# Optimization experiments

Hardware: AMD Instinct MI355X
Metric: run time of the kernel (lower is better)

## Reference

```python
import jax, jax.numpy as jnp
import numpy as np

D_MODEL = 1024
HEADS = 4
HDIM = 64


def setup_inputs() -> dict:
    key = jax.random.key(0)
    k_x, k_qw, k_qb, k_kw, k_kb, k_hw = jax.random.split(key, 6)
    hidden_states = jax.random.normal(k_x, (2, 4096, D_MODEL), dtype=jnp.float32)
    # xavier_uniform bound for Linear(d_model -> heads*hdim)
    fan_out = HEADS * HDIM
    bound = float(np.sqrt(6.0 / (D_MODEL + fan_out)))
    q_weight = jax.random.uniform(k_qw, (fan_out, D_MODEL), minval=-bound, maxval=bound, dtype=jnp.float32)
    k_weight = jax.random.uniform(k_kw, (fan_out, D_MODEL), minval=-bound, maxval=bound, dtype=jnp.float32)
    # nn.Linear default bias init: U(-1/sqrt(fan_in), 1/sqrt(fan_in))
    b_bound = float(1.0 / np.sqrt(D_MODEL))
    q_bias = jax.random.uniform(k_qb, (fan_out,), minval=-b_bound, maxval=b_bound, dtype=jnp.float32)
    k_bias = jax.random.uniform(k_kb, (fan_out,), minval=-b_bound, maxval=b_bound, dtype=jnp.float32)
    indexer_weights = jax.random.normal(k_hw, (HEADS,), dtype=jnp.float32) * 0.1
    return {
        "hidden_states": hidden_states,
        "q_weight": q_weight,
        "q_bias": q_bias,
        "k_weight": k_weight,
        "k_bias": k_bias,
        "indexer_weights": indexer_weights,
    }


def reference(hidden_states, q_weight, q_bias, k_weight, k_bias, indexer_weights):
    b, s, _ = hidden_states.shape
    # Linear projections: x @ W^T + b  -> [b, s, heads*hdim]
    q = hidden_states @ q_weight.T + q_bias
    k = hidden_states @ k_weight.T + k_bias
    q = q.reshape(b, s, HEADS, HDIM)  # [b, s, h, d]
    k = k.reshape(b, s, HEADS, HDIM)
    # per-head QK^T -> [b, h, s, s]
    scores = jnp.einsum("bqhd,bkhd->bhqk", q, k)
    scores = jax.nn.relu(scores)
    # weighted sum over heads -> [b, s, s]
    index_scores = jnp.einsum("bhqk,h->bqk", scores, indexer_weights)
    return index_scores
```

## Files before the change

kernel.cpp:

```cpp
#include <hip/hip_runtime.h>


typedef __bf16 bf16;
typedef __bf16 bf16x4 __attribute__((ext_vector_type(4)));
typedef __bf16 bf16x8 __attribute__((ext_vector_type(8)));
typedef float f32x4 __attribute__((ext_vector_type(4)));

#define NB 2
#define SEQ 4096
#define DMODEL 1024
#define NHEAD 4
#define HDIM 64
#define NPROJ 256
#define MTOT 8192

__device__ __forceinline__ void async16(const void* g, void* l) {
  __builtin_amdgcn_global_load_lds(
      (const __attribute__((address_space(1))) void*)g,
      (__attribute__((address_space(3))) void*)l, 16, 0, 0);
}

__global__ __launch_bounds__(256) void k_convert(const float* __restrict__ wq,
                                                 const float* __restrict__ wk,
                                                 bf16* __restrict__ wqb,
                                                 bf16* __restrict__ wkb) {
  int i = blockIdx.x * 256 + threadIdx.x;
  float4 a = ((const float4*)wq)[i];
  bf16x4 oa = {(bf16)a.x, (bf16)a.y, (bf16)a.z, (bf16)a.w};
  ((bf16x4*)wqb)[i] = oa;
  float4 b = ((const float4*)wk)[i];
  bf16x4 ob = {(bf16)b.x, (bf16)b.y, (bf16)b.z, (bf16)b.w};
  ((bf16x4*)wkb)[i] = ob;
}

__global__ __launch_bounds__(256, 4) void k_proj(
    const float* __restrict__ x, const bf16* __restrict__ wqb,
    const bf16* __restrict__ wkb, const float* __restrict__ qbias,
    const float* __restrict__ kbias, bf16* __restrict__ Qb,
    bf16* __restrict__ Kb) {
  __shared__ __align__(16) bf16 As[64 * 72];
  __shared__ __align__(16) bf16 Bs[128 * 64];
  const int t = threadIdx.x;
  const int lane = t & 63, w = t >> 6;
  const int m16 = lane & 15, q = lane >> 4;
  const int m0 = blockIdx.x * 64;
  const int z = blockIdx.y;
  const int nh = blockIdx.z;
  const bf16* __restrict__ W = z ? wkb : wqb;

  f32x4 acc[4][2];
#pragma unroll
  for (int i = 0; i < 4; i++)
#pragma unroll
    for (int j = 0; j < 2; j++) acc[i][j] = {0.f, 0.f, 0.f, 0.f};

  for (int kt = 0; kt < 16; kt++) {
#pragma unroll
    for (int p = 0; p < 4; p++) {
      int n0 = w * 32 + p * 8;
      int r = n0 + (lane >> 3);
      int c = (lane & 7) ^ (r & 7);
      async16(W + (size_t)(nh * 128 + r) * DMODEL + kt * 64 + c * 8,
              Bs + n0 * 64);
    }
#pragma unroll
    for (int p = 0; p < 4; p++) {
      int r = p * 16 + (t >> 4);
      int c = (t & 15) * 4;
      float4 v = *(const float4*)(x + (size_t)(m0 + r) * DMODEL + kt * 64 + c);
      bf16x4 o = {(bf16)v.x, (bf16)v.y, (bf16)v.z, (bf16)v.w};
      *(bf16x4*)(As + r * 72 + c) = o;
    }
    __builtin_amdgcn_s_waitcnt(0);
    __syncthreads();

#pragma unroll
    for (int s = 0; s < 2; s++) {
      bf16x8 a[4], b[2];
#pragma unroll
      for (int mt = 0; mt < 4; mt++)
        a[mt] = *(const bf16x8*)(As + (mt * 16 + m16) * 72 + s * 32 + q * 8);
#pragma unroll
      for (int nt = 0; nt < 2; nt++) {
        int n = w * 32 + nt * 16 + m16;
        int cc = (4 * s + q) ^ (n & 7);
        b[nt] = *(const bf16x8*)(Bs + n * 64 + cc * 8);
      }
#pragma unroll
      for (int mt = 0; mt < 4; mt++)
#pragma unroll
        for (int nt = 0; nt < 2; nt++)
          acc[mt][nt] = __builtin_amdgcn_mfma_f32_16x16x32_bf16(
              a[mt], b[nt], acc[mt][nt], 0, 0, 0);
    }
    __syncthreads();
  }

  const float* __restrict__ bias = z ? kbias : qbias;
  bf16* __restrict__ outp = z ? Kb : Qb;
#pragma unroll
  for (int nt = 0; nt < 2; nt++) {
    int col = nh * 128 + w * 32 + nt * 16 + m16;
    float bv = bias[col];
#pragma unroll
    for (int mt = 0; mt < 4; mt++) {
      int row0 = m0 + mt * 16 + q * 4;
#pragma unroll
      for (int e = 0; e < 4; e++)
        outp[(size_t)(row0 + e) * NPROJ + col] = (bf16)(acc[mt][nt][e] + bv);
    }
  }
}

__global__ __launch_bounds__(256, 2) void k_scores(
    const bf16* __restrict__ Qb, const bf16* __restrict__ Kb,
    const float* __restrict__ iw, float* __restrict__ out) {
  __shared__ __align__(16) bf16 Qs[16 * 2 * 512];
  __shared__ __align__(16) bf16 Ks[16 * 2 * 512];
  const int t = threadIdx.x;
  const int lane = t & 63, w = t >> 6;
  const int m16 = lane & 15, q = lane >> 4;

  const int L = blockIdx.x;
  const int xcd = L & 7;
  const int slot = L >> 3;
  const int row = xcd * 8 + (slot >> 5);
  const int kx = slot & 31;
  const int bz = row >> 5;
  const int qy = row & 31;

  const int rh = (w >> 1) * 64, ch = (w & 1) * 64;

  f32x4 accf[4][4];
#pragma unroll
  for (int i = 0; i < 4; i++)
#pragma unroll
    for (int j = 0; j < 4; j++) accf[i][j] = {0.f, 0.f, 0.f, 0.f};

  const size_t qbase = ((size_t)bz * SEQ + (size_t)qy * 128) * NPROJ;
  const size_t kbase = ((size_t)bz * SEQ + (size_t)kx * 128) * NPROJ;

  for (int hp = 0; hp < 2; hp++) {
#pragma unroll
    for (int p = 0; p < 8; p++) {
      int idx = w * 8 + p;
      int g = idx >> 1, hh = idx & 1;
      int r = g * 8 + (lane >> 3);
      int c = (lane & 7) ^ (r & 7);
      size_t src = (size_t)r * NPROJ + (hp * 2 + hh) * 64 + c * 8;
      async16(Qb + qbase + src, Qs + idx * 512);
      async16(Kb + kbase + src, Ks + idx * 512);
    }
    __builtin_amdgcn_s_waitcnt(0);
    __syncthreads();

#pragma unroll
    for (int hh = 0; hh < 2; hh++) {
      float wh = iw[hp * 2 + hh];
      bf16x8 b0[4], b1[4];
#pragma unroll
      for (int nt = 0; nt < 4; nt++) {
        int n = ch + nt * 16 + m16;
        const bf16* kb_ = Ks + (n >> 3) * 1024 + hh * 512 + (n & 7) * 64;
        b0[nt] = *(const bf16x8*)(kb_ + ((q) ^ (n & 7)) * 8);
        b1[nt] = *(const bf16x8*)(kb_ + ((4 + q) ^ (n & 7)) * 8);
      }
#pragma unroll
      for (int mt = 0; mt < 4; mt++) {
        int m = rh + mt * 16 + m16;
        const bf16* qa = Qs + (m >> 3) * 1024 + hh * 512 + (m & 7) * 64;
        bf16x8 a0 = *(const bf16x8*)(qa + ((q) ^ (m & 7)) * 8);
        bf16x8 a1 = *(const bf16x8*)(qa + ((4 + q) ^ (m & 7)) * 8);
#pragma unroll
        for (int nt = 0; nt < 4; nt++) {
          f32x4 tacc = {0.f, 0.f, 0.f, 0.f};
          tacc = __builtin_amdgcn_mfma_f32_16x16x32_bf16(a0, b0[nt], tacc, 0, 0, 0);
          tacc = __builtin_amdgcn_mfma_f32_16x16x32_bf16(a1, b1[nt], tacc, 0, 0, 0);
#pragma unroll
          for (int e = 0; e < 4; e++)
            accf[mt][nt][e] += wh * fmaxf(tacc[e], 0.f);
        }
      }
    }
    __syncthreads();
  }

#pragma unroll
  for (int mt = 0; mt < 4; mt++)
#pragma unroll
    for (int e = 0; e < 4; e++) {
      int r = qy * 128 + rh + mt * 16 + q * 4 + e;
      size_t ob = ((size_t)bz * SEQ + r) * SEQ + (size_t)kx * 128 + ch;
#pragma unroll
      for (int nt = 0; nt < 4; nt++)
        out[ob + nt * 16 + m16] = accf[mt][nt][e];
    }
}

extern "C" void kernel_launch(void* const* d_in, const int* in_sizes, int n_in,
                              void* d_out, int out_size, void* d_ws, size_t ws_size,
                              hipStream_t stream) {
  const float* x  = (const float*)d_in[0];
  const float* wq = (const float*)d_in[1];
  const float* qb = (const float*)d_in[2];
  const float* wk = (const float*)d_in[3];
  const float* kb = (const float*)d_in[4];
  const float* iw = (const float*)d_in[5];
  float* out = (float*)d_out;

  char* ws = (char*)d_ws;
  bf16* wqb = (bf16*)ws;
  bf16* wkb = (bf16*)(ws + 524288);
  bf16* Qb  = (bf16*)(ws + 1048576);
  bf16* Kb  = (bf16*)(ws + 1048576 + 4194304);

  k_convert<<<256, 256, 0, stream>>>(wq, wk, wqb, wkb);
  k_proj<<<dim3(128, 2, 2), 256, 0, stream>>>(x, wqb, wkb, qb, kb, Qb, Kb);
  k_scores<<<2048, 256, 0, stream>>>(Qb, Kb, iw, out);
}
```

Before: 202.6 us.

## Keep Q tile in registers and loop over four K tiles per block

The scores kernel now loads each wave's 32 query rows for all four heads straight into registers once. Each block then iterates over four 128-key tiles, staging every K tile (all heads, 128x256 bf16) in LDS with a 32-way XOR swizzle. The grid drops from 2048 to 512 blocks, and each wave computes a 32x128 output slice. This removes repeated Q staging and the per-head-pair LDS round trips, at the cost of higher register pressure, a 64KB LDS footprint that may cut occupancy, and no overlap between K loads and compute.

```diff
diff --git a/kernel.cpp b/kernel.cpp
--- a/kernel.cpp
+++ b/kernel.cpp
@@ -115,86 +115,93 @@
 __global__ __launch_bounds__(256, 2) void k_scores(
     const bf16* __restrict__ Qb, const bf16* __restrict__ Kb,
     const float* __restrict__ iw, float* __restrict__ out) {
-  __shared__ __align__(16) bf16 Qs[16 * 2 * 512];
-  __shared__ __align__(16) bf16 Ks[16 * 2 * 512];
+  __shared__ __align__(16) bf16 Ks[128 * 256];
   const int t = threadIdx.x;
   const int lane = t & 63, w = t >> 6;
   const int m16 = lane & 15, q = lane >> 4;
 
-  const int L = blockIdx.x;
-  const int xcd = L & 7;
-  const int slot = L >> 3;
-  const int row = xcd * 8 + (slot >> 5);
-  const int kx = slot & 31;
-  const int bz = row >> 5;
-  const int qy = row & 31;
-
-  const int rh = (w >> 1) * 64, ch = (w & 1) * 64;
-
-  f32x4 accf[4][4];
-#pragma unroll
-  for (int i = 0; i < 4; i++)
-#pragma unroll
-    for (int j = 0; j < 4; j++) accf[i][j] = {0.f, 0.f, 0.f, 0.f};
-
-  const size_t qbase = ((size_t)bz * SEQ + (size_t)qy * 128) * NPROJ;
-  const size_t kbase = ((size_t)bz * SEQ + (size_t)kx * 128) * NPROJ;
-
-  for (int hp = 0; hp < 2; hp++) {
-#pragma unroll
-    for (int p = 0; p < 8; p++) {
-      int idx = w * 8 + p;
-      int g = idx >> 1, hh = idx & 1;
-      int r = g * 8 + (lane >> 3);
-      int c = (lane & 7) ^ (r & 7);
-      size_t src = (size_t)r * NPROJ + (hp * 2 + hh) * 64 + c * 8;
-      async16(Qb + qbase + src, Qs + idx * 512);
-      async16(Kb + kbase + src, Ks + idx * 512);
+  const int bx = blockIdx.x;
+  const int kq = bx & 7;
+  const int strip = bx >> 3;
+  const int bz = strip >> 5;
+  const int q0 = (strip & 31) * 128;
+
+  const float wh0 = iw[0], wh1 = iw[1], wh2 = iw[2], wh3 = iw[3];
+  const float whs[4] = {wh0, wh1, wh2, wh3};
+
+  bf16x8 aq[2][4][2];
+  {
+    const bf16* qp =
+        Qb + (size_t)(bz * SEQ + q0 + w * 32 + m16) * NPROJ + q * 8;
+#pragma unroll
+    for (int mt = 0; mt < 2; mt++)
+#pragma unroll
+      for (int h = 0; h < 4; h++)
+#pragma unroll
+        for (int j = 0; j < 2; j++)
+          aq[mt][h][j] =
+              *(const bf16x8*)(qp + (size_t)mt * 16 * NPROJ + h * 64 + j * 32);
+  }
+
+  for (int i = 0; i < 4; i++) {
+    const int kx = kq * 4 + i;
+    const size_t kbase = ((size_t)bz * SEQ + (size_t)kx * 128) * NPROJ;
+    __syncthreads();
+#pragma unroll
+    for (int p = 0; p < 16; p++) {
+      int g = w * 16 + p;
+      int r = g * 2 + (lane >> 5);
+      int c = (lane & 31) ^ (r & 31);
+      async16(Kb + kbase + (size_t)r * NPROJ + c * 8, Ks + g * 512);
     }
     __builtin_amdgcn_s_waitcnt(0);
     __syncthreads();
 
-#pragma unroll
-    for (int hh = 0; hh < 2; hh++) {
-      float wh = iw[hp * 2 + hh];
-      bf16x8 b0[4], b1[4];
-#pragma unroll
-      for (int nt = 0; nt < 4; nt++) {
-        int n = ch + nt * 16 + m16;
-        const bf16* kb_ = Ks + (n >> 3) * 1024 + hh * 512 + (n & 7) * 64;
-        b0[nt] = *(const bf16x8*)(kb_ + ((q) ^ (n & 7)) * 8);
-        b1[nt] = *(const bf16x8*)(kb_ + ((4 + q) ^ (n & 7)) * 8);
+    f32x4 accf[2][8];
+#pragma unroll
+    for (int mt = 0; mt < 2; mt++)
+#pragma unroll
+      for (int nt = 0; nt < 8; nt++) accf[mt][nt] = {0.f, 0.f, 0.f, 0.f};
+
+#pragma unroll
+    for (int h = 0; h < 4; h++) {
+      const float wh = whs[h];
+      bf16x8 bk[8][2];
+#pragma unroll
+      for (int nt = 0; nt < 8; nt++) {
+        int n = nt * 16 + m16;
+        const bf16* kb_ = Ks + (size_t)n * 256;
+        int c0 = (h * 8 + q) ^ (n & 31);
+        int c1 = (h * 8 + 4 + q) ^ (n & 31);
+        bk[nt][0] = *(const bf16x8*)(kb_ + c0 * 8);
+        bk[nt][1] = *(const bf16x8*)(kb_ + c1 * 8);
       }
 #pragma unroll
-      for (int mt = 0; mt < 4; mt++) {
-        int m = rh + mt * 16 + m16;
-        const bf16* qa = Qs + (m >> 3) * 1024 + hh * 512 + (m & 7) * 64;
-        bf16x8 a0 = *(const bf16x8*)(qa + ((q) ^ (m & 7)) * 8);
-        bf16x8 a1 = *(const bf16x8*)(qa + ((4 + q) ^ (m & 7)) * 8);
-#pragma unroll
-        for (int nt = 0; nt < 4; nt++) {
+      for (int mt = 0; mt < 2; mt++)
+#pragma unroll
+        for (int nt = 0; nt < 8; nt++) {
           f32x4 tacc = {0.f, 0.f, 0.f, 0.f};
-          tacc = __builtin_amdgcn_mfma_f32_16x16x32_bf16(a0, b0[nt], tacc, 0, 0, 0);
-          tacc = __builtin_amdgcn_mfma_f32_16x16x32_bf16(a1, b1[nt], tacc, 0, 0, 0);
+          tacc = __builtin_amdgcn_mfma_f32_16x16x32_bf16(aq[mt][h][0], bk[nt][0],
+                                                         tacc, 0, 0, 0);
+          tacc = __builtin_amdgcn_mfma_f32_16x16x32_bf16(aq[mt][h][1], bk[nt][1],
+                                                         tacc, 0, 0, 0);
 #pragma unroll
           for (int e = 0; e < 4; e++)
             accf[mt][nt][e] += wh * fmaxf(tacc[e], 0.f);
         }
+    }
+
+#pragma unroll
+    for (int mt = 0; mt < 2; mt++)
+#pragma unroll
+      for (int e = 0; e < 4; e++) {
+        int r = q0 + w * 32 + mt * 16 + q * 4 + e;
+        size_t ob = ((size_t)bz * SEQ + r) * SEQ + (size_t)kx * 128;
+#pragma unroll
+        for (int nt = 0; nt < 8; nt++)
+          out[ob + nt * 16 + m16] = accf[mt][nt][e];
       }
-    }
-    __syncthreads();
-  }
-
-#pragma unroll
-  for (int mt = 0; mt < 4; mt++)
-#pragma unroll
-    for (int e = 0; e < 4; e++) {
-      int r = qy * 128 + rh + mt * 16 + q * 4 + e;
-      size_t ob = ((size_t)bz * SEQ + r) * SEQ + (size_t)kx * 128 + ch;
-#pragma unroll
-      for (int nt = 0; nt < 4; nt++)
-        out[ob + nt * 16 + m16] = accf[mt][nt][e];
-    }
+  }
 }
 
 extern "C" void kernel_launch(void* const* d_in, const int* in_sizes, int n_in,
@@ -216,5 +223,5 @@
 
   k_convert<<<256, 256, 0, stream>>>(wq, wk, wqb, wkb);
   k_proj<<<dim3(128, 2, 2), 256, 0, stream>>>(x, wqb, wkb, qb, kb, Qb, Kb);
-  k_scores<<<2048, 256, 0, stream>>>(Qb, Kb, iw, out);
-}
+  k_scores<<<512, 256, 0, stream>>>(Qb, Kb, iw, out);
+}
```

Measured after the change: 195.8 us. 3.3% less time.
